# Performance work log

Hardware: AMD Instinct MI355X
Metric: run time of the kernel (lower is better)

The kernel has to match this reference:

```python
import jax, jax.numpy as jnp
import numpy as np

IN_DIM = 64
OUT_DIM = 64
ATTN_DIM = 5
N_REL = 200
N_ENT = 40000
N_NODE = 500000
N_EDGE = 1000000
BATCH = 32


def setup_inputs() -> dict:
    key = jax.random.key(0)
    ks = jax.random.split(key, 20)
    n_rel_emb = 2 * N_REL + 1
    # forward args
    q_sub = jax.random.randint(ks[0], (BATCH,), 0, N_ENT)
    q_rel = jax.random.randint(ks[1], (BATCH,), 0, n_rel_emb)
    hidden = jax.random.normal(ks[2], (N_NODE, IN_DIM), dtype=jnp.float32)
    # edges columns: 0=batch idx, 1=unused, 2=rel, 3=unused, 4=sub, 5=obj
    e_batch = jax.random.randint(ks[3], (N_EDGE,), 0, BATCH)
    e_rel = jax.random.randint(ks[4], (N_EDGE,), 0, n_rel_emb)
    e_sub = jax.random.randint(ks[5], (N_EDGE,), 0, N_NODE)
    e_obj = jax.random.randint(ks[6], (N_EDGE,), 0, N_NODE)
    edges = jnp.stack([e_batch, e_batch, e_rel, e_rel, e_sub, e_obj], axis=1)
    nodes = jnp.stack([jax.random.randint(ks[7], (N_NODE,), 0, BATCH),
                       jax.random.randint(ks[8], (N_NODE,), 0, N_ENT)], axis=1)
    old_nodes_new_idx = jax.random.randint(ks[9], (100000,), 0, N_NODE)
    # parameters (stored as [in, out]; torch Linear does x @ W.T + b)
    def lin(k, fan_in, fan_out):
        b = 1.0 / np.sqrt(fan_in)
        return jax.random.uniform(k, (fan_in, fan_out), jnp.float32, -b, b)
    rela_embed = jax.random.normal(ks[10], (n_rel_emb, IN_DIM), dtype=jnp.float32)
    return {
        "hidden": hidden,
        "rela_embed": rela_embed,
        "Ws": lin(ks[11], IN_DIM, ATTN_DIM),
        "Wr": lin(ks[12], IN_DIM, ATTN_DIM),
        "Wqr_w": lin(ks[13], IN_DIM, ATTN_DIM),
        "Wqr_b": jnp.zeros((ATTN_DIM,), jnp.float32),
        "walpha_w": lin(ks[14], ATTN_DIM, 1),
        "walpha_b": jnp.zeros((1,), jnp.float32),
        "Wh": lin(ks[15], IN_DIM, OUT_DIM),
        "attn_fc_w": lin(ks[16], 2 * OUT_DIM, 1),
        "attn_fc_b": jnp.zeros((1,), jnp.float32),
        "Wnode_w": lin(ks[17], OUT_DIM, OUT_DIM),
        "Wnode_b": jnp.zeros((OUT_DIM,), jnp.float32),
        "q_sub": q_sub,
        "q_rel": q_rel,
        "edges": edges,
        "nodes": nodes,
        "old_nodes_new_idx": old_nodes_new_idx,
        "batchsize": BATCH,
    }


def reference(hidden, rela_embed, Ws, Wr, Wqr_w, Wqr_b, walpha_w, walpha_b,
              Wh, attn_fc_w, attn_fc_b, Wnode_w, Wnode_b,
              q_sub, q_rel, edges, nodes, old_nodes_new_idx, batchsize):
    n_node = nodes.shape[0]
    r_idx, rel, sub, obj = edges[:, 0], edges[:, 2], edges[:, 4], edges[:, 5]
    hs = hidden[sub]                      # [E, in_dim] gather
    hr = rela_embed[rel]                  # [E, in_dim]
    h_qr = rela_embed[q_rel][r_idx]       # [E, in_dim]
    message = hs - hr                     # [E, in_dim]
    attn = jax.nn.relu(hs @ Ws + hr @ Wr + h_qr @ Wqr_w + Wqr_b)   # [E, attn_dim]
    alpha = jax.nn.sigmoid(attn @ walpha_w + walpha_b)             # [E, 1]
    message = alpha * message
    # scatter-max over obj; empty segments filled with 0 (torch_scatter semantics)
    agg = jax.ops.segment_max(message, obj, num_segments=n_node)   # [n_node, in_dim]
    agg = jnp.where(jnp.isneginf(agg), 0.0, agg)
    hidden_new = agg @ Wh                 # act = identity        [n_node, out_dim]
    # edge attention over new node states
    cat = jnp.concatenate([hidden_new[sub], hidden_new[obj]], axis=-1)  # [E, 2*out]
    scores = jax.nn.leaky_relu((cat @ attn_fc_w + attn_fc_b)[:, 0], 0.2)  # [E]
    # source code overwrites scatter_softmax with a global softmax over all edges
    w = jax.nn.softmax(scores)            # [E]
    msg2 = w[:, None] * (hidden_new[obj] @ Wnode_w + Wnode_b)      # [E, out_dim]
    hidden_new = jax.ops.segment_sum(msg2, sub, num_segments=n_node)
    return hidden_new
```

## Files before the change

kernel.cpp:

```cpp
#include <hip/hip_runtime.h>
#include <math.h>
#include <float.h>


#define SCAN_BLK 256
#define SCAN_ITEMS 4
#define SCAN_CHUNK (SCAN_BLK * SCAN_ITEMS)
#define SOFT_G 2048
#define NPW 8
#define ONB 128

__global__ void k_tables(const float* __restrict__ rela, const float* __restrict__ Wr,
                         const float* __restrict__ Wqr_w, const float* __restrict__ Wqr_b,
                         const int* __restrict__ q_rel,
                         float* __restrict__ s2, float* __restrict__ s3,
                         int nrel, int batch) {
  int tid = blockIdx.x * blockDim.x + threadIdx.x;
  int stride = gridDim.x * blockDim.x;
  for (int idx = tid; idx < nrel * 5; idx += stride) {
    int r = idx / 5, j = idx % 5;
    float acc = 0.f;
    for (int k = 0; k < 64; k++) acc += rela[r * 64 + k] * Wr[k * 5 + j];
    s2[idx] = acc;
  }
  for (int idx = tid; idx < batch * 5; idx += stride) {
    int b = idx / 5, j = idx % 5;
    int qr = q_rel[b];
    float acc = Wqr_b[j];
    for (int k = 0; k < 64; k++) acc += rela[qr * 64 + k] * Wqr_w[k * 5 + j];
    s3[idx] = acc;
  }
}

__global__ void k_fuse(const float* __restrict__ Wh, const float* __restrict__ Wn,
                       float* __restrict__ W2) {
  int tid = threadIdx.x;
  for (int idx = tid; idx < 64 * 64; idx += 256) {
    int k = idx >> 6, m = idx & 63;
    float acc = 0.f;
    for (int j = 0; j < 64; j++) acc += Wh[k * 64 + j] * Wn[j * 64 + m];
    W2[idx] = acc;
  }
}

__global__ void __launch_bounds__(256, 2)
k_proj(const float* __restrict__ hidden, const float* __restrict__ Ws_g,
       float* __restrict__ P, int N) {
  int n = blockIdx.x * blockDim.x + threadIdx.x;
  if (n >= N) return;
  float hs[64];
  const float4* h4 = (const float4*)(hidden + (size_t)n * 64);
#pragma unroll
  for (int k4 = 0; k4 < 16; k4++) {
    float4 h = h4[k4];
    hs[k4 * 4 + 0] = h.x; hs[k4 * 4 + 1] = h.y; hs[k4 * 4 + 2] = h.z; hs[k4 * 4 + 3] = h.w;
  }
  float acc[5] = {0.f, 0.f, 0.f, 0.f, 0.f};
#pragma unroll
  for (int k = 0; k < 64; k++) {
    float h = hs[k];
#pragma unroll
    for (int j = 0; j < 5; j++) acc[j] += h * Ws_g[k * 5 + j];
  }
#pragma unroll
  for (int j = 0; j < 5; j++) P[(size_t)n * 5 + j] = acc[j];
}

__global__ void k_hist(const int* __restrict__ edges, int* __restrict__ cnt, int E, int N) {
  int e = blockIdx.x * blockDim.x + threadIdx.x;
  if (e < E) {
    int sub = edges[e * 6 + 4];
    int obj = edges[e * 6 + 5];
    atomicAdd(&cnt[obj], 1);
    atomicAdd(&cnt[N + sub], 1);
  }
}

__global__ void k_scan_partial(const int* __restrict__ cnt, int* __restrict__ part, int n) {
  __shared__ int sdata[SCAN_BLK];
  int base = blockIdx.x * SCAN_CHUNK + threadIdx.x * SCAN_ITEMS;
  int s = 0;
#pragma unroll
  for (int j = 0; j < SCAN_ITEMS; j++) { int i = base + j; if (i < n) s += cnt[i]; }
  sdata[threadIdx.x] = s;
  __syncthreads();
  for (int d = SCAN_BLK / 2; d > 0; d >>= 1) {
    if (threadIdx.x < d) sdata[threadIdx.x] += sdata[threadIdx.x + d];
    __syncthreads();
  }
  if (threadIdx.x == 0) part[blockIdx.x] = sdata[0];
}

__global__ void k_scan_top(int* part, int nblk) {
  __shared__ int lds[1024];
  int tid = threadIdx.x;
  int v = (tid < nblk) ? part[tid] : 0;
  lds[tid] = v;
  __syncthreads();
  for (int d = 1; d < 1024; d <<= 1) {
    int t = (tid >= d) ? lds[tid - d] : 0;
    __syncthreads();
    lds[tid] += t;
    __syncthreads();
  }
  if (tid < nblk) part[tid] = lds[tid] - v;
}

__global__ void k_scan_final(const int* __restrict__ cnt, const int* __restrict__ part,
                             int* __restrict__ off, int n) {
  __shared__ int lds[SCAN_BLK];
  int tid = threadIdx.x;
  int base = blockIdx.x * SCAN_CHUNK + tid * SCAN_ITEMS;
  int c[SCAN_ITEMS];
  int s = 0;
#pragma unroll
  for (int j = 0; j < SCAN_ITEMS; j++) { int i = base + j; c[j] = (i < n) ? cnt[i] : 0; s += c[j]; }
  int v = s;
  lds[tid] = s;
  __syncthreads();
  for (int d = 1; d < SCAN_BLK; d <<= 1) {
    int t = (tid >= d) ? lds[tid - d] : 0;
    __syncthreads();
    lds[tid] += t;
    __syncthreads();
  }
  int run = part[blockIdx.x] + (lds[tid] - v);
#pragma unroll
  for (int j = 0; j < SCAN_ITEMS; j++) { int i = base + j; if (i < n) off[i] = run; run += c[j]; }
}

__global__ void k_scatter(const int* __restrict__ edges, const float* __restrict__ P,
                          const float* __restrict__ s2, const float* __restrict__ s3,
                          const float* __restrict__ walpha_w, const float* __restrict__ walpha_b,
                          int* __restrict__ cur, int4* __restrict__ rec_obj,
                          int2* __restrict__ rec_sub, int E, int N) {
  int e = blockIdx.x * blockDim.x + threadIdx.x;
  if (e >= E) return;
  int ridx = edges[e * 6 + 0];
  int rel  = edges[e * 6 + 2];
  int sub  = edges[e * 6 + 4];
  int obj  = edges[e * 6 + 5];
  float z = walpha_b[0];
#pragma unroll
  for (int j = 0; j < 5; j++) {
    float vj = P[(size_t)sub * 5 + j] + s2[rel * 5 + j] + s3[ridx * 5 + j];
    z += fmaxf(vj, 0.f) * walpha_w[j];
  }
  float a = 1.f / (1.f + expf(-z));
  int p = atomicAdd(&cur[obj], 1);
  rec_obj[p] = make_int4(sub, rel, __float_as_int(a), 0);
  int q = atomicAdd(&cur[N + sub], 1) - E;
  rec_sub[q] = make_int2(obj, sub);
}

__global__ void k_agg(const int* __restrict__ off, const int4* __restrict__ rec_obj,
                      const float* __restrict__ hidden, const float* __restrict__ rela,
                      float* __restrict__ agg, int N) {
  int lane = threadIdx.x & 63;
  int wid  = blockIdx.x * (blockDim.x >> 6) + (threadIdx.x >> 6);
  int node0 = wid * NPW;
  if (node0 >= N) return;
  int ov = 0;
  if (lane <= NPW) {
    int idx = node0 + lane;
    if (idx > N) idx = N;
    ov = off[idx];
  }
  int B   = __shfl(ov, 0);
  int End = __shfl(ov, NPW);
  int lbase = B;
  int rx = 0, ry = 0; float rz = 0.f;
  {
    int p = lbase + lane;
    if (p < End) { int4 r = rec_obj[p]; rx = r.x; ry = r.y; rz = __int_as_float(r.z); }
  }
  int cur = B;
  for (int i = 0; i < NPW; i++) {
    int node = node0 + i;
    if (node >= N) break;
    int en = __shfl(ov, i + 1);
    int bst = cur;
    float vmax = -FLT_MAX;
    while (cur < en) {
      int idx = cur - lbase;
      if (idx >= 64) {
        lbase += 64;
        int p = lbase + lane;
        if (p < End) { int4 r = rec_obj[p]; rx = r.x; ry = r.y; rz = __int_as_float(r.z); }
        idx = 0;
      }
      int sub = __shfl(rx, idx);
      int rel = __shfl(ry, idx);
      float a = __shfl(rz, idx);
      float x = a * (hidden[(size_t)sub * 64 + lane] - rela[rel * 64 + lane]);
      vmax = fmaxf(vmax, x);
      cur++;
    }
    agg[(size_t)node * 64 + lane] = (en > bst) ? vmax : 0.f;
  }
}

__global__ void __launch_bounds__(256, 2)
k_uv(const float* __restrict__ A, const float* __restrict__ W, const float* __restrict__ fw,
     float* __restrict__ u, float* __restrict__ v, int N) {
  int n = blockIdx.x * blockDim.x + threadIdx.x;
  if (n >= N) return;
  float a[64];
  const float4* A4 = (const float4*)(A + (size_t)n * 64);
#pragma unroll
  for (int k4 = 0; k4 < 16; k4++) {
    float4 h = A4[k4];
    a[k4 * 4 + 0] = h.x; a[k4 * 4 + 1] = h.y; a[k4 * 4 + 2] = h.z; a[k4 * 4 + 3] = h.w;
  }
  float acc[64];
#pragma unroll
  for (int j = 0; j < 64; j++) acc[j] = 0.f;
#pragma unroll
  for (int k = 0; k < 64; k++) {
    float ak = a[k];
#pragma unroll
    for (int j = 0; j < 64; j++) acc[j] += ak * W[k * 64 + j];
  }
  float uacc = 0.f, vacc = 0.f;
#pragma unroll
  for (int j = 0; j < 64; j++) {
    uacc += acc[j] * fw[j];
    vacc += acc[j] * fw[64 + j];
  }
  u[n] = uacc;
  v[n] = vacc;
}

__global__ void k_scores(const int2* __restrict__ rec_sub, const float* __restrict__ u,
                         const float* __restrict__ v, const float* __restrict__ fb,
                         float* __restrict__ scores, float* __restrict__ pmax,
                         float* __restrict__ psum, int E) {
  __shared__ float red_m[256], red_s[256];
  float b = fb[0];
  float lm = -FLT_MAX, ls = 0.f;
  for (int pos = blockIdx.x * blockDim.x + threadIdx.x; pos < E; pos += gridDim.x * blockDim.x) {
    int2 r = rec_sub[pos];
    float s = u[r.y] + v[r.x] + b;
    s = (s >= 0.f) ? s : 0.2f * s;
    scores[pos] = s;
    if (s > lm) { ls = ls * expf(lm - s) + 1.f; lm = s; }
    else        { ls += expf(s - lm); }
  }
  red_m[threadIdx.x] = lm; red_s[threadIdx.x] = ls;
  __syncthreads();
  for (int d = blockDim.x / 2; d > 0; d >>= 1) {
    if (threadIdx.x < d) {
      float m1 = red_m[threadIdx.x], s1 = red_s[threadIdx.x];
      float m2 = red_m[threadIdx.x + d], s2 = red_s[threadIdx.x + d];
      float m = fmaxf(m1, m2);
      float s = 0.f;
      if (m > -FLT_MAX) s = s1 * expf(m1 - m) + s2 * expf(m2 - m);
      red_m[threadIdx.x] = m; red_s[threadIdx.x] = s;
    }
    __syncthreads();
  }
  if (threadIdx.x == 0) { pmax[blockIdx.x] = red_m[0]; psum[blockIdx.x] = red_s[0]; }
}

__global__ void k_softmax_final(const float* __restrict__ pmax, const float* __restrict__ psum,
                                float* __restrict__ scal, int G) {
  __shared__ float red_m[256], red_s[256];
  float lm = -FLT_MAX, ls = 0.f;
  for (int i = threadIdx.x; i < G; i += 256) {
    float m2 = pmax[i], s2 = psum[i];
    if (m2 > lm) { ls = ls * expf(lm - m2) + s2; lm = m2; }
    else         { ls += s2 * expf(m2 - lm); }
  }
  red_m[threadIdx.x] = lm; red_s[threadIdx.x] = ls;
  __syncthreads();
  for (int d = 128; d > 0; d >>= 1) {
    if (threadIdx.x < d) {
      float m1 = red_m[threadIdx.x], s1 = red_s[threadIdx.x];
      float m2 = red_m[threadIdx.x + d], s2 = red_s[threadIdx.x + d];
      float m = fmaxf(m1, m2);
      float s = 0.f;
      if (m > -FLT_MAX) s = s1 * expf(m1 - m) + s2 * expf(m2 - m);
      red_m[threadIdx.x] = m; red_s[threadIdx.x] = s;
    }
    __syncthreads();
  }
  if (threadIdx.x == 0) { scal[0] = red_m[0]; scal[1] = red_s[0]; }
}

__global__ void k_expw(float* __restrict__ scores, const float* __restrict__ scal, int E) {
  int i = blockIdx.x * blockDim.x + threadIdx.x;
  if (i < E) scores[i] = expf(scores[i] - scal[0]);
}

__global__ void k_aggsum(const int* __restrict__ off, const int2* __restrict__ rec_sub,
                         const float* __restrict__ wexp, const float* __restrict__ agg,
                         float* __restrict__ t, float* __restrict__ wsum, int N, int E) {
  int lane = threadIdx.x & 63;
  int wid  = blockIdx.x * (blockDim.x >> 6) + (threadIdx.x >> 6);
  int node0 = wid * NPW;
  if (node0 >= N) return;
  int ov = 0;
  if (lane <= NPW) {
    int idx = node0 + lane;
    ov = (idx >= N) ? E : (off[N + idx] - E);
  }
  int B   = __shfl(ov, 0);
  int End = __shfl(ov, NPW);
  int lbase = B;
  int objr = 0; float wr = 0.f;
  {
    int p = lbase + lane;
    if (p < End) { objr = rec_sub[p].x; wr = wexp[p]; }
  }
  int cur = B;
  for (int i = 0; i < NPW; i++) {
    int node = node0 + i;
    if (node >= N) break;
    int en = __shfl(ov, i + 1);
    float acc = 0.f, wa = 0.f;
    while (cur < en) {
      int idx = cur - lbase;
      if (idx >= 64) {
        lbase += 64;
        int p = lbase + lane;
        if (p < End) { objr = rec_sub[p].x; wr = wexp[p]; }
        idx = 0;
      }
      int obj = __shfl(objr, idx);
      float ww = __shfl(wr, idx);
      acc += ww * agg[(size_t)obj * 64 + lane];
      wa  += ww;
      cur++;
    }
    t[(size_t)node * 64 + lane] = acc;
    if (lane == 0) wsum[node] = wa;
  }
}

__global__ void __launch_bounds__(ONB)
k_mm_out(const float* __restrict__ W2, const float* __restrict__ bias,
         const float* __restrict__ wsum, const float* __restrict__ scal,
         float* C, int N) {
  __shared__ float lds[ONB * 64];
  int tid = threadIdx.x;
  int n0 = blockIdx.x * ONB;
  int n = n0 + tid;
  float inv = 1.f / scal[1];
  if (n < N) {
    float a[64];
    const float4* A4 = (const float4*)(C + (size_t)n * 64);
#pragma unroll
    for (int q = 0; q < 16; q++) {
      float4 h = A4[q];
      a[q * 4 + 0] = h.x; a[q * 4 + 1] = h.y; a[q * 4 + 2] = h.z; a[q * 4 + 3] = h.w;
    }
    float wsn = wsum[n];
    float acc[64];
#pragma unroll
    for (int j = 0; j < 64; j++) acc[j] = wsn * bias[j];
#pragma unroll
    for (int k = 0; k < 64; k++) {
      float ak = a[k];
#pragma unroll
      for (int j = 0; j < 64; j++) acc[j] += ak * W2[k * 64 + j];
    }
#pragma unroll
    for (int g = 0; g < 16; g++) {
      int pos = g ^ (tid & 15);
      *(float4*)&lds[tid * 64 + pos * 4] =
          make_float4(acc[g * 4] * inv, acc[g * 4 + 1] * inv,
                      acc[g * 4 + 2] * inv, acc[g * 4 + 3] * inv);
    }
  }
  __syncthreads();
  float4* Cg = (float4*)(C + (size_t)n0 * 64);
#pragma unroll
  for (int i = 0; i < 16; i++) {
    int f = tid + ONB * i;
    int row = f >> 4, c4 = f & 15;
    if (n0 + row < N) {
      int pos = c4 ^ (row & 15);
      Cg[f] = *(float4*)&lds[row * 64 + pos * 4];
    }
  }
}

extern "C" void kernel_launch(void* const* d_in, const int* in_sizes, int n_in,
                              void* d_out, int out_size, void* d_ws, size_t ws_size,
                              hipStream_t stream) {
  const float* hidden    = (const float*)d_in[0];
  const float* rela      = (const float*)d_in[1];
  const float* Ws        = (const float*)d_in[2];
  const float* Wr        = (const float*)d_in[3];
  const float* Wqr_w     = (const float*)d_in[4];
  const float* Wqr_b     = (const float*)d_in[5];
  const float* walpha_w  = (const float*)d_in[6];
  const float* walpha_b  = (const float*)d_in[7];
  const float* Wh        = (const float*)d_in[8];
  const float* attn_fc_w = (const float*)d_in[9];
  const float* attn_fc_b = (const float*)d_in[10];
  const float* Wnode_w   = (const float*)d_in[11];
  const float* Wnode_b   = (const float*)d_in[12];
  const int*   q_rel     = (const int*)d_in[14];
  const int*   edges     = (const int*)d_in[15];

  int N = in_sizes[0] / 64;
  int E = in_sizes[15] / 6;
  int nrel = in_sizes[1] / 64;
  int batch = in_sizes[14];

  char* w = (char*)d_ws;
  size_t o = 0;
  #define WS_ALLOC(ptr_t, name, bytes) \
    ptr_t name = (ptr_t)(w + o); o = (o + (size_t)(bytes) + 255) & ~(size_t)255;
  WS_ALLOC(float*, aggT,    (size_t)N * 64 * 4)
  WS_ALLOC(float*, P,       (size_t)N * 5 * 4)
  WS_ALLOC(int4*,  rec_obj, (size_t)E * 16)
  WS_ALLOC(int2*,  rec_sub, (size_t)E * 8)
  WS_ALLOC(int*,   cnt,     (size_t)2 * N * 4)
  WS_ALLOC(int*,   off,     (size_t)2 * N * 4)
  WS_ALLOC(float*, wsum,    (size_t)N * 4)
  WS_ALLOC(int*,   part,    1024 * 4)
  WS_ALLOC(float*, pmax,    SOFT_G * 4)
  WS_ALLOC(float*, psum,    SOFT_G * 4)
  WS_ALLOC(float*, s2t,     (size_t)nrel * 5 * 4)
  WS_ALLOC(float*, s3t,     (size_t)batch * 5 * 4)
  WS_ALLOC(float*, scal,    2 * 4)
  WS_ALLOC(float*, W2,      64 * 64 * 4)
  #undef WS_ALLOC

  float* u = P;
  float* v = P + N;
  float* scores = (float*)cnt;
  float* tbuf = (float*)d_out;

  k_tables<<<16, 256, 0, stream>>>(rela, Wr, Wqr_w, Wqr_b, q_rel, s2t, s3t, nrel, batch);
  k_fuse<<<1, 256, 0, stream>>>(Wh, Wnode_w, W2);
  k_proj<<<(N + 255) / 256, 256, 0, stream>>>(hidden, Ws, P, N);
  hipMemsetAsync(cnt, 0, (size_t)2 * N * 4, stream);
  k_hist<<<(E + 255) / 256, 256, 0, stream>>>(edges, cnt, E, N);
  int SCAN_N = 2 * N;
  int nblk = (SCAN_N + SCAN_CHUNK - 1) / SCAN_CHUNK;
  k_scan_partial<<<nblk, SCAN_BLK, 0, stream>>>(cnt, part, SCAN_N);
  k_scan_top<<<1, 1024, 0, stream>>>(part, nblk);
  k_scan_final<<<nblk, SCAN_BLK, 0, stream>>>(cnt, part, off, SCAN_N);
  hipMemcpyAsync(cnt, off, (size_t)2 * N * 4, hipMemcpyDeviceToDevice, stream);
  k_scatter<<<(E + 255) / 256, 256, 0, stream>>>(edges, P, s2t, s3t, walpha_w, walpha_b,
                                                 cnt, rec_obj, rec_sub, E, N);
  int csr_blocks = (N + NPW * 4 - 1) / (NPW * 4);
  k_agg<<<csr_blocks, 256, 0, stream>>>(off, rec_obj, hidden, rela, aggT, N);
  k_uv<<<(N + 255) / 256, 256, 0, stream>>>(aggT, Wh, attn_fc_w, u, v, N);
  k_scores<<<SOFT_G, 256, 0, stream>>>(rec_sub, u, v, attn_fc_b, scores, pmax, psum, E);
  k_softmax_final<<<1, 256, 0, stream>>>(pmax, psum, scal, SOFT_G);
  k_expw<<<(E + 255) / 256, 256, 0, stream>>>(scores, scal, E);
  k_aggsum<<<csr_blocks, 256, 0, stream>>>(off, rec_sub, scores , aggT, tbuf, wsum, N, E);
  k_mm_out<<<(N + ONB - 1) / ONB, ONB, 0, stream>>>(W2, Wnode_b, wsum, scal, (float*)d_out, N);
}
```

Measured before the change: 887.1 us.

## Apply fused node transform before edge aggregation and fold u/v projection

Computes u and v directly from the aggregated features using precomputed Wh·attn_fc vectors, so the 64x64 matmul in the old u/v kernel is dropped. The same kernel transforms agg by W2 (Wh·Wnode) in place before the weighted sum. The final output matmul kernel and the wsum buffer are removed, and bias and normalisation are applied inside the aggregation. This moves the dense matmul from post-aggregation to pre-aggregation, relying on linearity, and removes one full pass over the N×64 buffer.

```diff
diff --git a/kernel.cpp b/kernel.cpp
--- a/kernel.cpp
+++ b/kernel.cpp
@@ -8,7 +8,6 @@
 #define SCAN_CHUNK (SCAN_BLK * SCAN_ITEMS)
 #define SOFT_G 2048
 #define NPW 8
-#define ONB 128
 
 __global__ void k_tables(const float* __restrict__ rela, const float* __restrict__ Wr,
                          const float* __restrict__ Wqr_w, const float* __restrict__ Wqr_b,
@@ -33,13 +32,20 @@
 }
 
 __global__ void k_fuse(const float* __restrict__ Wh, const float* __restrict__ Wn,
-                       float* __restrict__ W2) {
+                       const float* __restrict__ fw,
+                       float* __restrict__ W2, float* __restrict__ fuv) {
   int tid = threadIdx.x;
   for (int idx = tid; idx < 64 * 64; idx += 256) {
     int k = idx >> 6, m = idx & 63;
     float acc = 0.f;
     for (int j = 0; j < 64; j++) acc += Wh[k * 64 + j] * Wn[j * 64 + m];
     W2[idx] = acc;
+  }
+  if (tid < 128) {
+    int k = tid & 63, h = tid >> 6;
+    float acc = 0.f;
+    for (int j = 0; j < 64; j++) acc += Wh[k * 64 + j] * fw[h * 64 + j];
+    fuv[h * 64 + k] = acc;
   }
 }
 
@@ -200,35 +206,63 @@
   }
 }
 
-__global__ void __launch_bounds__(256, 2)
-k_uv(const float* __restrict__ A, const float* __restrict__ W, const float* __restrict__ fw,
-     float* __restrict__ u, float* __restrict__ v, int N) {
-  int n = blockIdx.x * blockDim.x + threadIdx.x;
-  if (n >= N) return;
-  float a[64];
-  const float4* A4 = (const float4*)(A + (size_t)n * 64);
-#pragma unroll
-  for (int k4 = 0; k4 < 16; k4++) {
-    float4 h = A4[k4];
-    a[k4 * 4 + 0] = h.x; a[k4 * 4 + 1] = h.y; a[k4 * 4 + 2] = h.z; a[k4 * 4 + 3] = h.w;
-  }
+__global__ void __launch_bounds__(128)
+k_trans(float* A, const float* __restrict__ W2, const float* __restrict__ fuv,
+        float* __restrict__ u, float* __restrict__ v, int N) {
+  __shared__ float lds[64 * 64];
+  int tid = threadIdx.x;
+  int n0 = blockIdx.x * 128;
+  int n = n0 + tid;
+  bool act = (n < N);
   float acc[64];
-#pragma unroll
-  for (int j = 0; j < 64; j++) acc[j] = 0.f;
-#pragma unroll
-  for (int k = 0; k < 64; k++) {
-    float ak = a[k];
-#pragma unroll
-    for (int j = 0; j < 64; j++) acc[j] += ak * W[k * 64 + j];
-  }
-  float uacc = 0.f, vacc = 0.f;
-#pragma unroll
-  for (int j = 0; j < 64; j++) {
-    uacc += acc[j] * fw[j];
-    vacc += acc[j] * fw[64 + j];
-  }
-  u[n] = uacc;
-  v[n] = vacc;
+  if (act) {
+    float a[64];
+    const float4* A4 = (const float4*)(A + (size_t)n * 64);
+#pragma unroll
+    for (int q = 0; q < 16; q++) {
+      float4 h = A4[q];
+      a[q * 4 + 0] = h.x; a[q * 4 + 1] = h.y; a[q * 4 + 2] = h.z; a[q * 4 + 3] = h.w;
+    }
+    float uacc = 0.f, vacc = 0.f;
+#pragma unroll
+    for (int k = 0; k < 64; k++) {
+      uacc += a[k] * fuv[k];
+      vacc += a[k] * fuv[64 + k];
+    }
+    u[n] = uacc;
+    v[n] = vacc;
+#pragma unroll
+    for (int j = 0; j < 64; j++) acc[j] = 0.f;
+#pragma unroll
+    for (int k = 0; k < 64; k++) {
+      float ak = a[k];
+#pragma unroll
+      for (int j = 0; j < 64; j++) acc[j] += ak * W2[k * 64 + j];
+    }
+  }
+  for (int ph = 0; ph < 2; ph++) {
+    if (act && (tid >> 6) == ph) {
+      int r = tid & 63;
+#pragma unroll
+      for (int g = 0; g < 16; g++) {
+        int pos = g ^ (tid & 15);
+        *(float4*)&lds[r * 64 + pos * 4] =
+            make_float4(acc[g * 4], acc[g * 4 + 1], acc[g * 4 + 2], acc[g * 4 + 3]);
+      }
+    }
+    __syncthreads();
+    float4* Cg = (float4*)(A + (size_t)(n0 + ph * 64) * 64);
+#pragma unroll
+    for (int i = 0; i < 8; i++) {
+      int f = tid + 128 * i;
+      int row = f >> 4, c4 = f & 15;
+      if (n0 + ph * 64 + row < N) {
+        int pos = c4 ^ (row & 15);
+        Cg[f] = *(float4*)&lds[row * 64 + pos * 4];
+      }
+    }
+    __syncthreads();
+  }
 }
 
 __global__ void k_scores(const int2* __restrict__ rec_sub, const float* __restrict__ u,
@@ -293,12 +327,15 @@
 }
 
 __global__ void k_aggsum(const int* __restrict__ off, const int2* __restrict__ rec_sub,
-                         const float* __restrict__ wexp, const float* __restrict__ agg,
-                         float* __restrict__ t, float* __restrict__ wsum, int N, int E) {
+                         const float* __restrict__ wexp, const float* __restrict__ agg2,
+                         const float* __restrict__ bias, const float* __restrict__ scal,
+                         float* __restrict__ out, int N, int E) {
   int lane = threadIdx.x & 63;
   int wid  = blockIdx.x * (blockDim.x >> 6) + (threadIdx.x >> 6);
   int node0 = wid * NPW;
   if (node0 >= N) return;
+  float bl = bias[lane];
+  float inv = 1.f / scal[1];
   int ov = 0;
   if (lane <= NPW) {
     int idx = node0 + lane;
@@ -328,60 +365,11 @@
       }
       int obj = __shfl(objr, idx);
       float ww = __shfl(wr, idx);
-      acc += ww * agg[(size_t)obj * 64 + lane];
+      acc += ww * agg2[(size_t)obj * 64 + lane];
       wa  += ww;
       cur++;
     }
-    t[(size_t)node * 64 + lane] = acc;
-    if (lane == 0) wsum[node] = wa;
-  }
-}
-
-__global__ void __launch_bounds__(ONB)
-k_mm_out(const float* __restrict__ W2, const float* __restrict__ bias,
-         const float* __restrict__ wsum, const float* __restrict__ scal,
-         float* C, int N) {
-  __shared__ float lds[ONB * 64];
-  int tid = threadIdx.x;
-  int n0 = blockIdx.x * ONB;
-  int n = n0 + tid;
-  float inv = 1.f / scal[1];
-  if (n < N) {
-    float a[64];
-    const float4* A4 = (const float4*)(C + (size_t)n * 64);
-#pragma unroll
-    for (int q = 0; q < 16; q++) {
-      float4 h = A4[q];
-      a[q * 4 + 0] = h.x; a[q * 4 + 1] = h.y; a[q * 4 + 2] = h.z; a[q * 4 + 3] = h.w;
-    }
-    float wsn = wsum[n];
-    float acc[64];
-#pragma unroll
-    for (int j = 0; j < 64; j++) acc[j] = wsn * bias[j];
-#pragma unroll
-    for (int k = 0; k < 64; k++) {
-      float ak = a[k];
-#pragma unroll
-      for (int j = 0; j < 64; j++) acc[j] += ak * W2[k * 64 + j];
-    }
-#pragma unroll
-    for (int g = 0; g < 16; g++) {
-      int pos = g ^ (tid & 15);
-      *(float4*)&lds[tid * 64 + pos * 4] =
-          make_float4(acc[g * 4] * inv, acc[g * 4 + 1] * inv,
-                      acc[g * 4 + 2] * inv, acc[g * 4 + 3] * inv);
-    }
-  }
-  __syncthreads();
-  float4* Cg = (float4*)(C + (size_t)n0 * 64);
-#pragma unroll
-  for (int i = 0; i < 16; i++) {
-    int f = tid + ONB * i;
-    int row = f >> 4, c4 = f & 15;
-    if (n0 + row < N) {
-      int pos = c4 ^ (row & 15);
-      Cg[f] = *(float4*)&lds[row * 64 + pos * 4];
-    }
+    out[(size_t)node * 64 + lane] = (acc + wa * bl) * inv;
   }
 }
 
@@ -419,7 +407,6 @@
   WS_ALLOC(int2*,  rec_sub, (size_t)E * 8)
   WS_ALLOC(int*,   cnt,     (size_t)2 * N * 4)
   WS_ALLOC(int*,   off,     (size_t)2 * N * 4)
-  WS_ALLOC(float*, wsum,    (size_t)N * 4)
   WS_ALLOC(int*,   part,    1024 * 4)
   WS_ALLOC(float*, pmax,    SOFT_G * 4)
   WS_ALLOC(float*, psum,    SOFT_G * 4)
@@ -427,15 +414,15 @@
   WS_ALLOC(float*, s3t,     (size_t)batch * 5 * 4)
   WS_ALLOC(float*, scal,    2 * 4)
   WS_ALLOC(float*, W2,      64 * 64 * 4)
+  WS_ALLOC(float*, fuv,     2 * 64 * 4)
   #undef WS_ALLOC
 
   float* u = P;
   float* v = P + N;
   float* scores = (float*)cnt;
-  float* tbuf = (float*)d_out;
 
   k_tables<<<16, 256, 0, stream>>>(rela, Wr, Wqr_w, Wqr_b, q_rel, s2t, s3t, nrel, batch);
-  k_fuse<<<1, 256, 0, stream>>>(Wh, Wnode_w, W2);
+  k_fuse<<<1, 256, 0, stream>>>(Wh, Wnode_w, attn_fc_w, W2, fuv);
   k_proj<<<(N + 255) / 256, 256, 0, stream>>>(hidden, Ws, P, N);
   hipMemsetAsync(cnt, 0, (size_t)2 * N * 4, stream);
   k_hist<<<(E + 255) / 256, 256, 0, stream>>>(edges, cnt, E, N);
@@ -449,10 +436,10 @@
                                                  cnt, rec_obj, rec_sub, E, N);
   int csr_blocks = (N + NPW * 4 - 1) / (NPW * 4);
   k_agg<<<csr_blocks, 256, 0, stream>>>(off, rec_obj, hidden, rela, aggT, N);
-  k_uv<<<(N + 255) / 256, 256, 0, stream>>>(aggT, Wh, attn_fc_w, u, v, N);
+  k_trans<<<(N + 127) / 128, 128, 0, stream>>>(aggT, W2, fuv, u, v, N);
   k_scores<<<SOFT_G, 256, 0, stream>>>(rec_sub, u, v, attn_fc_b, scores, pmax, psum, E);
   k_softmax_final<<<1, 256, 0, stream>>>(pmax, psum, scal, SOFT_G);
   k_expw<<<(E + 255) / 256, 256, 0, stream>>>(scores, scal, E);
-  k_aggsum<<<csr_blocks, 256, 0, stream>>>(off, rec_sub, scores , aggT, tbuf, wsum, N, E);
-  k_mm_out<<<(N + ONB - 1) / ONB, ONB, 0, stream>>>(W2, Wnode_b, wsum, scal, (float*)d_out, N);
-}
+  k_aggsum<<<csr_blocks, 256, 0, stream>>>(off, rec_sub, scores , aggT ,
+                                           Wnode_b, scal, (float*)d_out, N, E);
+}
```

Result: faster. 784.8 us (-11.5%).
